# Kernel optimization log

Measured on AMD Instinct MI355X. Metric: run time of the kernel, lower is better.

## Reference

```python
import jax, jax.numpy as jnp
import numpy as np

GROUP_SIZE = 128  # infeatures // n_groups = 4096 // 32


def setup_inputs() -> dict:
    key = jax.random.key(0)
    k1, k2, k3, k4 = jax.random.split(key, 4)
    M, K, N = 256, 4096, 4096
    n_groups = K // GROUP_SIZE  # 32
    A = jax.random.normal(k1, (M, K), dtype=jnp.float32)
    # uint4 quantized weights, stored unpacked as int32 in [0, 16)
    qweight = jax.random.randint(k2, (N, K), 0, 16, dtype=jnp.int32)
    scales = jax.random.uniform(k3, (N, n_groups), dtype=jnp.float32) * 0.05 + 1e-3
    zeros = jax.random.uniform(k4, (N, n_groups), dtype=jnp.float32) * 15.0
    return {"A": A, "qweight": qweight, "scales": scales, "zeros": zeros}


def reference(A, qweight, scales, zeros):
    # Fused dequant + GEMM: W[n,k] = (q[n,k] - zeros[n, k//G]) * scales[n, k//G]
    N, K = qweight.shape
    s = jnp.repeat(scales, GROUP_SIZE, axis=1)   # [N, K]
    z = jnp.repeat(zeros, GROUP_SIZE, axis=1)    # [N, K]
    W = (qweight.astype(A.dtype) - z) * s        # dequantized weight [N, K]
    # Linear: Y = A @ W^T  -> [M, N]
    return jnp.einsum('mk,nk->mn', A, W)
```

## Files before the change

### kernel.cpp

```cpp
#include <hip/hip_runtime.h>

typedef __attribute__((ext_vector_type(8))) short bf16x8;
typedef __attribute__((ext_vector_type(4))) float f32x4;

#define MDIM 256
#define NDIM 4096
#define KDIM 4096
#define KP8 (KDIM / 8)
#define NGRP 32
#define BM 128
#define BN 32
#define BK 64
#define SPLITK 2
#define KLOC (KDIM / SPLITK)
#define NTL (KLOC / BK)

typedef const __attribute__((address_space(1))) void* gas_ptr;
typedef __attribute__((address_space(3))) void* las_ptr;

__device__ __forceinline__ unsigned short f2bf(float f) {
  union { float f; unsigned int u; } v;
  v.f = f;
  unsigned int r = v.u + 0x7FFFu + ((v.u >> 16) & 1u);
  return (unsigned short)(r >> 16);
}

__device__ __forceinline__ void gl_lds16(const void* g, void* l) {
  __builtin_amdgcn_global_load_lds((gas_ptr)g, (las_ptr)l, 16, 0, 0);
}

__global__ void prep_kernel(const float* __restrict__ A, const int* __restrict__ q,
                            unsigned short* __restrict__ Ab,
                            unsigned int* __restrict__ qp) {
  int i = blockIdx.x * 256 + threadIdx.x;
  if (i < NDIM * KP8) {
    const int4* p = reinterpret_cast<const int4*>(q) + (size_t)i * 2;
    int4 a = p[0], b = p[1];
    unsigned int d = (unsigned)(a.x & 15) | ((unsigned)(a.y & 15) << 4) |
                     ((unsigned)(a.z & 15) << 8) | ((unsigned)(a.w & 15) << 12) |
                     ((unsigned)(b.x & 15) << 16) | ((unsigned)(b.y & 15) << 20) |
                     ((unsigned)(b.z & 15) << 24) | ((unsigned)(b.w & 15) << 28);
    qp[i] = d;
  } else {
    int j = i - NDIM * KP8;
    float4 v = reinterpret_cast<const float4*>(A)[j];
    ushort4 o;
    o.x = f2bf(v.x); o.y = f2bf(v.y); o.z = f2bf(v.z); o.w = f2bf(v.w);
    reinterpret_cast<ushort4*>(Ab)[j] = o;
  }
}

__global__ void convA_kernel(const float* __restrict__ A,
                             unsigned short* __restrict__ Ab) {
  int i = blockIdx.x * 256 + threadIdx.x;
  float4 v = reinterpret_cast<const float4*>(A)[i];
  ushort4 o;
  o.x = f2bf(v.x); o.y = f2bf(v.y); o.z = f2bf(v.z); o.w = f2bf(v.w);
  reinterpret_cast<ushort4*>(Ab)[i] = o;
}

__global__ __launch_bounds__(256, 2) void gemm_pk(
    const unsigned short* __restrict__ Ab, const unsigned int* __restrict__ qp,
    const float* __restrict__ sc, const float* __restrict__ zr,
    float* __restrict__ out) {
  __shared__ __align__(16) unsigned short A_lds[4][BM * BK];
  __shared__ __align__(16) unsigned short W_lds[2][BN * BK];
  __shared__ float s_lds[BN * 16];
  __shared__ float zs_lds[BN * 16];

  const int tid = threadIdx.x;
  const int lane = tid & 63;
  const int wave = tid >> 6;
  const int wm = wave >> 1;
  const int wn = wave & 1;

  const int bid = blockIdx.x;
  const int x = bid & 7;
  const int j = bid >> 3;
  const int r = x * 16 + (j >> 2);
  const int c = j & 3;
  const int m0 = (c & 1) * BM;
  const int ks = c >> 1;
  const int n0 = r * BN;

  for (int i = tid; i < BN * 16; i += 256) {
    int n = i >> 4;
    int g16 = i & 15;
    float s = sc[(size_t)(n0 + n) * NGRP + ks * 16 + g16];
    float z = zr[(size_t)(n0 + n) * NGRP + ks * 16 + g16];
    s_lds[i] = s;
    zs_lds[i] = z * s;
  }

  const unsigned short* Abase = Ab + (size_t)m0 * KDIM + ks * KLOC;
  const int wrow = tid >> 3;
  const int wc = tid & 7;
  const unsigned int* qpbase =
      qp + (size_t)(n0 + wrow) * KP8 + ks * (KLOC / 8) + wc;

  unsigned int qd[4];

  auto loadW = [&](int t, int idx) { qd[idx] = qpbase[t * 8]; };
  auto stageA = [&](int t, int b) {
#pragma unroll
    for (int i = 0; i < 4; ++i) {
      int cid = i * 256 + tid;
      int row = cid >> 3;
      int cp = cid & 7;
      int cs = cp ^ (row & 7);
      const unsigned short* g = Abase + (size_t)row * KDIM + t * BK + cs * 8;
      gl_lds16(g, &A_lds[b][(i * 256 + wave * 64) * 8]);
    }
  };
  auto writeW = [&](int t, int b, int idx) {
    int gg = t >> 1;
    float s = s_lds[wrow * 16 + gg];
    float zs = zs_lds[wrow * 16 + gg];
    unsigned int d = qd[idx];
    bf16x8 w;
#pragma unroll
    for (int jj = 0; jj < 8; ++jj)
      w[jj] = (short)f2bf(fmaf((float)((d >> (4 * jj)) & 15u), s, -zs));
    *reinterpret_cast<bf16x8*>(
        &W_lds[b][wrow * BK + ((wc ^ (wrow & 7)) << 3)]) = w;
  };

  f32x4 acc[4];
#pragma unroll
  for (int i = 0; i < 4; ++i) acc[i] = (f32x4){0.f, 0.f, 0.f, 0.f};

  const int l15 = lane & 15;
  const int lhi = lane >> 4;
  const int ar0 = wm * 64 + l15;
  const int asw = ar0 & 7;
  const int br = wn * 16 + l15;
  const int bsw = br & 7;

  auto compute = [&](int ab, int wb) {
#pragma unroll
    for (int kss = 0; kss < 2; ++kss) {
      bf16x8 bfr = *reinterpret_cast<const bf16x8*>(
          &W_lds[wb][br * BK + ((((kss << 2) + lhi) ^ bsw) << 3)]);
#pragma unroll
      for (int mi = 0; mi < 4; ++mi) {
        bf16x8 afr = *reinterpret_cast<const bf16x8*>(
            &A_lds[ab][(ar0 + mi * 16) * BK + ((((kss << 2) + lhi) ^ asw) << 3)]);
        acc[mi] = __builtin_amdgcn_mfma_f32_16x16x32_bf16(afr, bfr, acc[mi], 0, 0, 0);
      }
    }
  };

  loadW(0, 0); stageA(0, 0);
  loadW(1, 1); stageA(1, 1);
  loadW(2, 2); stageA(2, 2);

  asm volatile("s_waitcnt lgkmcnt(0)" ::: "memory");
  __builtin_amdgcn_s_barrier();
  __builtin_amdgcn_sched_barrier(0);
  writeW(0, 0, 0);
  asm volatile("s_waitcnt vmcnt(10) lgkmcnt(0)" ::: "memory");
  __builtin_amdgcn_s_barrier();
  __builtin_amdgcn_sched_barrier(0);

  for (int tb = 0; tb < NTL; tb += 4) {
#pragma unroll
    for (int u = 0; u < 4; ++u) {
      const int t = tb + u;
      const int tp = (t + 3 < NTL) ? (t + 3) : 0;
      loadW(tp, (u + 3) & 3);
      stageA(tp, (u + 3) & 3);
      compute(u, u & 1);
      if (t + 1 < NTL) writeW(t + 1, (u + 1) & 1, (u + 1) & 3);
      asm volatile("s_waitcnt vmcnt(10) lgkmcnt(0)" ::: "memory");
      __builtin_amdgcn_s_barrier();
      __builtin_amdgcn_sched_barrier(0);
    }
  }

  const int col = n0 + wn * 16 + l15;
  const int rb = m0 + wm * 64 + (lhi << 2);
#pragma unroll
  for (int mi = 0; mi < 4; ++mi)
#pragma unroll
    for (int jj = 0; jj < 4; ++jj)
      unsafeAtomicAdd(&out[(size_t)(rb + mi * 16 + jj) * NDIM + col],
                      acc[mi][jj]);
}

__global__ __launch_bounds__(256, 2) void gemm_r3(
    const unsigned short* __restrict__ Ab, const int* __restrict__ qw,
    const float* __restrict__ sc, const float* __restrict__ zr,
    float* __restrict__ out) {
  __shared__ __align__(16) unsigned short A_lds[4][BM * BK];
  __shared__ __align__(16) unsigned short W_lds[2][BN * BK];
  __shared__ float s_lds[BN * 16];
  __shared__ float zs_lds[BN * 16];

  const int tid = threadIdx.x;
  const int lane = tid & 63;
  const int wave = tid >> 6;
  const int wm = wave >> 1;
  const int wn = wave & 1;

  const int bid = blockIdx.x;
  const int x = bid & 7;
  const int j = bid >> 3;
  const int r = x * 16 + (j >> 2);
  const int c = j & 3;
  const int m0 = (c & 1) * BM;
  const int ks = c >> 1;
  const int n0 = r * BN;

  for (int i = tid; i < BN * 16; i += 256) {
    int n = i >> 4;
    int g16 = i & 15;
    float s = sc[(size_t)(n0 + n) * NGRP + ks * 16 + g16];
    float z = zr[(size_t)(n0 + n) * NGRP + ks * 16 + g16];
    s_lds[i] = s;
    zs_lds[i] = z * s;
  }

  const unsigned short* Abase = Ab + (size_t)m0 * KDIM + ks * KLOC;
  const int wrow = tid >> 3;
  const int wc = tid & 7;
  const int* qbase = qw + (size_t)(n0 + wrow) * KDIM + ks * KLOC + wc * 8;

  int4 qr[4][2];

  auto loadW = [&](int t, int idx) {
    const int* p = qbase + t * BK;
    qr[idx][0] = *reinterpret_cast<const int4*>(p);
    qr[idx][1] = *reinterpret_cast<const int4*>(p + 4);
  };
  auto stageA = [&](int t, int b) {
#pragma unroll
    for (int i = 0; i < 4; ++i) {
      int cid = i * 256 + tid;
      int row = cid >> 3;
      int cp = cid & 7;
      int cs = cp ^ (row & 7);
      const unsigned short* g = Abase + (size_t)row * KDIM + t * BK + cs * 8;
      gl_lds16(g, &A_lds[b][(i * 256 + wave * 64) * 8]);
    }
  };
  auto writeW = [&](int t, int b, int idx) {
    int gg = t >> 1;
    float s = s_lds[wrow * 16 + gg];
    float zs = zs_lds[wrow * 16 + gg];
    int q[8] = {qr[idx][0].x, qr[idx][0].y, qr[idx][0].z, qr[idx][0].w,
                qr[idx][1].x, qr[idx][1].y, qr[idx][1].z, qr[idx][1].w};
    bf16x8 w;
#pragma unroll
    for (int jj = 0; jj < 8; ++jj)
      w[jj] = (short)f2bf(fmaf((float)q[jj], s, -zs));
    *reinterpret_cast<bf16x8*>(
        &W_lds[b][wrow * BK + ((wc ^ (wrow & 7)) << 3)]) = w;
  };

  f32x4 acc[4];
#pragma unroll
  for (int i = 0; i < 4; ++i) acc[i] = (f32x4){0.f, 0.f, 0.f, 0.f};

  const int l15 = lane & 15;
  const int lhi = lane >> 4;
  const int ar0 = wm * 64 + l15;
  const int asw = ar0 & 7;
  const int br = wn * 16 + l15;
  const int bsw = br & 7;

  auto compute = [&](int ab, int wb) {
#pragma unroll
    for (int kss = 0; kss < 2; ++kss) {
      bf16x8 bfr = *reinterpret_cast<const bf16x8*>(
          &W_lds[wb][br * BK + ((((kss << 2) + lhi) ^ bsw) << 3)]);
#pragma unroll
      for (int mi = 0; mi < 4; ++mi) {
        bf16x8 afr = *reinterpret_cast<const bf16x8*>(
            &A_lds[ab][(ar0 + mi * 16) * BK + ((((kss << 2) + lhi) ^ asw) << 3)]);
        acc[mi] = __builtin_amdgcn_mfma_f32_16x16x32_bf16(afr, bfr, acc[mi], 0, 0, 0);
      }
    }
  };

  loadW(0, 0); stageA(0, 0);
  loadW(1, 1); stageA(1, 1);
  loadW(2, 2); stageA(2, 2);

  asm volatile("s_waitcnt lgkmcnt(0)" ::: "memory");
  __builtin_amdgcn_s_barrier();
  __builtin_amdgcn_sched_barrier(0);
  writeW(0, 0, 0);
  asm volatile("s_waitcnt vmcnt(12) lgkmcnt(0)" ::: "memory");
  __builtin_amdgcn_s_barrier();
  __builtin_amdgcn_sched_barrier(0);

  for (int tb = 0; tb < NTL; tb += 4) {
#pragma unroll
    for (int u = 0; u < 4; ++u) {
      const int t = tb + u;
      const int tp = (t + 3 < NTL) ? (t + 3) : 0;
      loadW(tp, (u + 3) & 3);
      stageA(tp, (u + 3) & 3);
      compute(u, u & 1);
      if (t + 1 < NTL) writeW(t + 1, (u + 1) & 1, (u + 1) & 3);
      asm volatile("s_waitcnt vmcnt(12) lgkmcnt(0)" ::: "memory");
      __builtin_amdgcn_s_barrier();
      __builtin_amdgcn_sched_barrier(0);
    }
  }

  const int col = n0 + wn * 16 + l15;
  const int rb = m0 + wm * 64 + (lhi << 2);
#pragma unroll
  for (int mi = 0; mi < 4; ++mi)
#pragma unroll
    for (int jj = 0; jj < 4; ++jj)
      unsafeAtomicAdd(&out[(size_t)(rb + mi * 16 + jj) * NDIM + col],
                      acc[mi][jj]);
}

extern "C" void kernel_launch(void* const* d_in, const int* in_sizes, int n_in,
                              void* d_out, int out_size, void* d_ws, size_t ws_size,
                              hipStream_t stream) {
  const float* A = (const float*)d_in[0];
  const int* qw = (const int*)d_in[1];
  const float* sc = (const float*)d_in[2];
  const float* zr = (const float*)d_in[3];
  float* out = (float*)d_out;

  hipMemsetAsync(d_out, 0, (size_t)MDIM * NDIM * sizeof(float), stream);

  if (ws_size >= (10u << 20)) {
    unsigned short* Ab = (unsigned short*)d_ws;
    unsigned int* qp = (unsigned int*)((char*)d_ws + (2u << 20));
    prep_kernel<<<9216, 256, 0, stream>>>(A, qw, Ab, qp);
    gemm_pk<<<(MDIM / BM) * (NDIM / BN) * SPLITK, 256, 0, stream>>>(
        Ab, qp, sc, zr, out);
  } else {
    unsigned short* Ab = (unsigned short*)d_ws;
    convA_kernel<<<(MDIM * KDIM / 4) / 256, 256, 0, stream>>>(A, Ab);
    gemm_r3<<<(MDIM / BM) * (NDIM / BN) * SPLITK, 256, 0, stream>>>(
        Ab, qw, sc, zr, out);
  }
}
```

Baseline: 134.5 us.

## Use 256x64 tiles with 512 threads and split-K of 4 in packed GEMM

Replaces the 128x32, 256-thread packed-weight GEMM with a 256x64 tile kernel that runs 512 threads and covers the full M dimension, using split-K of 4. Each wave now computes two N subtiles, so every A fragment loaded from LDS is reused across more MFMAs. Dequantized weights are shared by all M rows, so they are computed once instead of twice. The cost is larger LDS use, fewer blocks (256), one block per CU, and twice as many atomic adds on the output from the extra split-K.

Result: faster. 129.6 us (-3.6%).

```diff
diff --git a/kernel.cpp b/kernel.cpp
--- a/kernel.cpp
+++ b/kernel.cpp
@@ -8,12 +8,6 @@
 #define KDIM 4096
 #define KP8 (KDIM / 8)
 #define NGRP 32
-#define BM 128
-#define BN 32
-#define BK 64
-#define SPLITK 2
-#define KLOC (KDIM / SPLITK)
-#define NTL (KLOC / BK)
 
 typedef const __attribute__((address_space(1))) void* gas_ptr;
 typedef __attribute__((address_space(3))) void* las_ptr;
@@ -50,23 +44,22 @@
   }
 }
 
-__global__ void convA_kernel(const float* __restrict__ A,
-                             unsigned short* __restrict__ Ab) {
-  int i = blockIdx.x * 256 + threadIdx.x;
-  float4 v = reinterpret_cast<const float4*>(A)[i];
-  ushort4 o;
-  o.x = f2bf(v.x); o.y = f2bf(v.y); o.z = f2bf(v.z); o.w = f2bf(v.w);
-  reinterpret_cast<ushort4*>(Ab)[i] = o;
-}
-
-__global__ __launch_bounds__(256, 2) void gemm_pk(
+#define BM 256
+#define BN 64
+#define BK 64
+#define SPLITK 4
+#define KLOC (KDIM / SPLITK)
+#define NTL (KLOC / BK)
+#define GPS (KLOC / 128)
+
+__global__ __launch_bounds__(512, 1) void gemm_big(
     const unsigned short* __restrict__ Ab, const unsigned int* __restrict__ qp,
     const float* __restrict__ sc, const float* __restrict__ zr,
     float* __restrict__ out) {
   __shared__ __align__(16) unsigned short A_lds[4][BM * BK];
   __shared__ __align__(16) unsigned short W_lds[2][BN * BK];
-  __shared__ float s_lds[BN * 16];
-  __shared__ float zs_lds[BN * 16];
+  __shared__ float s_lds[BN * GPS];
+  __shared__ float zs_lds[BN * GPS];
 
   const int tid = threadIdx.x;
   const int lane = tid & 63;
@@ -75,28 +68,25 @@
   const int wn = wave & 1;
 
   const int bid = blockIdx.x;
-  const int x = bid & 7;
+  const int xcd = bid & 7;
   const int j = bid >> 3;
-  const int r = x * 16 + (j >> 2);
-  const int c = j & 3;
-  const int m0 = (c & 1) * BM;
-  const int ks = c >> 1;
-  const int n0 = r * BN;
-
-  for (int i = tid; i < BN * 16; i += 256) {
-    int n = i >> 4;
-    int g16 = i & 15;
-    float s = sc[(size_t)(n0 + n) * NGRP + ks * 16 + g16];
-    float z = zr[(size_t)(n0 + n) * NGRP + ks * 16 + g16];
-    s_lds[i] = s;
-    zs_lds[i] = z * s;
-  }
-
-  const unsigned short* Abase = Ab + (size_t)m0 * KDIM + ks * KLOC;
+  const int ks = j >> 3;
+  const int nl = j & 7;
+  const int n0 = (xcd * 8 + nl) * BN;
+  const int kbase = ks * KLOC;
+
+  {
+    int n = tid >> 3, g = tid & 7;
+    float s = sc[(size_t)(n0 + n) * NGRP + ks * GPS + g];
+    float z = zr[(size_t)(n0 + n) * NGRP + ks * GPS + g];
+    s_lds[tid] = s;
+    zs_lds[tid] = z * s;
+  }
+
+  const unsigned short* Abase = Ab + kbase;
   const int wrow = tid >> 3;
   const int wc = tid & 7;
-  const unsigned int* qpbase =
-      qp + (size_t)(n0 + wrow) * KP8 + ks * (KLOC / 8) + wc;
+  const unsigned int* qpbase = qp + (size_t)(n0 + wrow) * KP8 + (kbase >> 3) + wc;
 
   unsigned int qd[4];
 
@@ -104,18 +94,18 @@
   auto stageA = [&](int t, int b) {
 #pragma unroll
     for (int i = 0; i < 4; ++i) {
-      int cid = i * 256 + tid;
+      int cid = i * 512 + tid;
       int row = cid >> 3;
       int cp = cid & 7;
       int cs = cp ^ (row & 7);
       const unsigned short* g = Abase + (size_t)row * KDIM + t * BK + cs * 8;
-      gl_lds16(g, &A_lds[b][(i * 256 + wave * 64) * 8]);
+      gl_lds16(g, &A_lds[b][(i * 512 + wave * 64) * 8]);
     }
   };
   auto writeW = [&](int t, int b, int idx) {
     int gg = t >> 1;
-    float s = s_lds[wrow * 16 + gg];
-    float zs = zs_lds[wrow * 16 + gg];
+    float s = s_lds[wrow * GPS + gg];
+    float zs = zs_lds[wrow * GPS + gg];
     unsigned int d = qd[idx];
     bf16x8 w;
 #pragma unroll
@@ -125,27 +115,33 @@
         &W_lds[b][wrow * BK + ((wc ^ (wrow & 7)) << 3)]) = w;
   };
 
-  f32x4 acc[4];
-#pragma unroll
-  for (int i = 0; i < 4; ++i) acc[i] = (f32x4){0.f, 0.f, 0.f, 0.f};
+  f32x4 acc[4][2];
+#pragma unroll
+  for (int i = 0; i < 4; ++i)
+#pragma unroll
+    for (int n = 0; n < 2; ++n) acc[i][n] = (f32x4){0.f, 0.f, 0.f, 0.f};
 
   const int l15 = lane & 15;
   const int lhi = lane >> 4;
   const int ar0 = wm * 64 + l15;
   const int asw = ar0 & 7;
-  const int br = wn * 16 + l15;
-  const int bsw = br & 7;
 
   auto compute = [&](int ab, int wb) {
 #pragma unroll
     for (int kss = 0; kss < 2; ++kss) {
-      bf16x8 bfr = *reinterpret_cast<const bf16x8*>(
-          &W_lds[wb][br * BK + ((((kss << 2) + lhi) ^ bsw) << 3)]);
-#pragma unroll
-      for (int mi = 0; mi < 4; ++mi) {
-        bf16x8 afr = *reinterpret_cast<const bf16x8*>(
-            &A_lds[ab][(ar0 + mi * 16) * BK + ((((kss << 2) + lhi) ^ asw) << 3)]);
-        acc[mi] = __builtin_amdgcn_mfma_f32_16x16x32_bf16(afr, bfr, acc[mi], 0, 0, 0);
+#pragma unroll
+      for (int ni = 0; ni < 2; ++ni) {
+        const int br = wn * 32 + ni * 16 + l15;
+        bf16x8 bfr = *reinterpret_cast<const bf16x8*>(
+            &W_lds[wb][br * BK + ((((kss << 2) + lhi) ^ (br & 7)) << 3)]);
+#pragma unroll
+        for (int mi = 0; mi < 4; ++mi) {
+          bf16x8 afr = *reinterpret_cast<const bf16x8*>(
+              &A_lds[ab][(ar0 + mi * 16) * BK +
+                         ((((kss << 2) + lhi) ^ asw) << 3)]);
+          acc[mi][ni] = __builtin_amdgcn_mfma_f32_16x16x32_bf16(
+              afr, bfr, acc[mi][ni], 0, 0, 0);
+        }
       }
     }
   };
@@ -177,24 +173,41 @@
     }
   }
 
-  const int col = n0 + wn * 16 + l15;
-  const int rb = m0 + wm * 64 + (lhi << 2);
+  const int col = n0 + wn * 32 + l15;
+  const int rb = wm * 64 + (lhi << 2);
 #pragma unroll
   for (int mi = 0; mi < 4; ++mi)
 #pragma unroll
-    for (int jj = 0; jj < 4; ++jj)
-      unsafeAtomicAdd(&out[(size_t)(rb + mi * 16 + jj) * NDIM + col],
-                      acc[mi][jj]);
+    for (int ni = 0; ni < 2; ++ni)
+#pragma unroll
+      for (int jj = 0; jj < 4; ++jj)
+        unsafeAtomicAdd(&out[(size_t)(rb + mi * 16 + jj) * NDIM + col + ni * 16],
+                        acc[mi][ni][jj]);
+}
+
+#define FBM 128
+#define FBN 32
+#define FSPLITK 2
+#define FKLOC (KDIM / FSPLITK)
+#define FNTL (FKLOC / BK)
+
+__global__ void convA_kernel(const float* __restrict__ A,
+                             unsigned short* __restrict__ Ab) {
+  int i = blockIdx.x * 256 + threadIdx.x;
+  float4 v = reinterpret_cast<const float4*>(A)[i];
+  ushort4 o;
+  o.x = f2bf(v.x); o.y = f2bf(v.y); o.z = f2bf(v.z); o.w = f2bf(v.w);
+  reinterpret_cast<ushort4*>(Ab)[i] = o;
 }
 
 __global__ __launch_bounds__(256, 2) void gemm_r3(
     const unsigned short* __restrict__ Ab, const int* __restrict__ qw,
     const float* __restrict__ sc, const float* __restrict__ zr,
     float* __restrict__ out) {
-  __shared__ __align__(16) unsigned short A_lds[4][BM * BK];
-  __shared__ __align__(16) unsigned short W_lds[2][BN * BK];
-  __shared__ float s_lds[BN * 16];
-  __shared__ float zs_lds[BN * 16];
+  __shared__ __align__(16) unsigned short A_lds[4][FBM * BK];
+  __shared__ __align__(16) unsigned short W_lds[2][FBN * BK];
+  __shared__ float s_lds[FBN * 16];
+  __shared__ float zs_lds[FBN * 16];
 
   const int tid = threadIdx.x;
   const int lane = tid & 63;
@@ -207,11 +220,11 @@
   const int j = bid >> 3;
   const int r = x * 16 + (j >> 2);
   const int c = j & 3;
-  const int m0 = (c & 1) * BM;
+  const int m0 = (c & 1) * FBM;
   const int ks = c >> 1;
-  const int n0 = r * BN;
-
-  for (int i = tid; i < BN * 16; i += 256) {
+  const int n0 = r * FBN;
+
+  for (int i = tid; i < FBN * 16; i += 256) {
     int n = i >> 4;
     int g16 = i & 15;
     float s = sc[(size_t)(n0 + n) * NGRP + ks * 16 + g16];
@@ -220,10 +233,10 @@
     zs_lds[i] = z * s;
   }
 
-  const unsigned short* Abase = Ab + (size_t)m0 * KDIM + ks * KLOC;
+  const unsigned short* Abase = Ab + (size_t)m0 * KDIM + ks * FKLOC;
   const int wrow = tid >> 3;
   const int wc = tid & 7;
-  const int* qbase = qw + (size_t)(n0 + wrow) * KDIM + ks * KLOC + wc * 8;
+  const int* qbase = qw + (size_t)(n0 + wrow) * KDIM + ks * FKLOC + wc * 8;
 
   int4 qr[4][2];
 
@@ -294,15 +307,15 @@
   __builtin_amdgcn_s_barrier();
   __builtin_amdgcn_sched_barrier(0);
 
-  for (int tb = 0; tb < NTL; tb += 4) {
+  for (int tb = 0; tb < FNTL; tb += 4) {
 #pragma unroll
     for (int u = 0; u < 4; ++u) {
       const int t = tb + u;
-      const int tp = (t + 3 < NTL) ? (t + 3) : 0;
+      const int tp = (t + 3 < FNTL) ? (t + 3) : 0;
       loadW(tp, (u + 3) & 3);
       stageA(tp, (u + 3) & 3);
       compute(u, u & 1);
-      if (t + 1 < NTL) writeW(t + 1, (u + 1) & 1, (u + 1) & 3);
+      if (t + 1 < FNTL) writeW(t + 1, (u + 1) & 1, (u + 1) & 3);
       asm volatile("s_waitcnt vmcnt(12) lgkmcnt(0)" ::: "memory");
       __builtin_amdgcn_s_barrier();
       __builtin_amdgcn_sched_barrier(0);
@@ -334,12 +347,11 @@
     unsigned short* Ab = (unsigned short*)d_ws;
     unsigned int* qp = (unsigned int*)((char*)d_ws + (2u << 20));
     prep_kernel<<<9216, 256, 0, stream>>>(A, qw, Ab, qp);
-    gemm_pk<<<(MDIM / BM) * (NDIM / BN) * SPLITK, 256, 0, stream>>>(
-        Ab, qp, sc, zr, out);
+    gemm_big<<<(NDIM / BN) * SPLITK, 512, 0, stream>>>(Ab, qp, sc, zr, out);
   } else {
     unsigned short* Ab = (unsigned short*)d_ws;
     convA_kernel<<<(MDIM * KDIM / 4) / 256, 256, 0, stream>>>(A, Ab);
-    gemm_r3<<<(MDIM / BM) * (NDIM / BN) * SPLITK, 256, 0, stream>>>(
+    gemm_r3<<<(MDIM / FBM) * (NDIM / FBN) * FSPLITK, 256, 0, stream>>>(
         Ab, qw, sc, zr, out);
   }
 }
```
